# Kernel tuning notes

Measured on AMD Instinct MI355X. Metric: run time of the kernel, lower is better.

## Reference

```python
import jax, jax.numpy as jnp
import numpy as np

N = 262144  # num_channels (o*i)
K = 5       # kernel_size


def setup_inputs() -> dict:
    key = jax.random.key(0)
    k1, k2, k3 = jax.random.split(key, 3)
    return {
        "input_filter": jax.random.normal(k1, (N, K, K, K), dtype=jnp.float32),
        "theta_v": jax.random.normal(k2, (N, 3), dtype=jnp.float32),
        "theta": jax.random.normal(k3, (N,), dtype=jnp.float32),
    }


def _rodrigues(theta_v, theta):
    # F.normalize(theta_v, p=2) with eps=1e-12
    norm = jnp.linalg.norm(theta_v, axis=-1, keepdims=True)
    v = theta_v / jnp.maximum(norm, 1e-12)
    vx, vy, vz = v[:, 0], v[:, 1], v[:, 2]
    z = jnp.zeros_like(vx)
    # skew-symmetric cross-product matrix m, shape (n,3,3)
    m = jnp.stack([z, -vz, vy,
                   vz, z, -vx,
                   -vy, vx, z], axis=-1).reshape(-1, 3, 3)
    s = jnp.sin(theta)[:, None, None]
    c = (1.0 - jnp.cos(theta))[:, None, None]
    I3 = jnp.eye(3, dtype=theta_v.dtype)
    return I3 + s * m + c * jnp.einsum('nij,njk->nik', m, m)


def _base_grid(k):
    # matches _get_base_grids: coord along axis i -> channel 0, j -> 1, l -> 2
    c = jnp.linspace(-1.0, 1.0, k, dtype=jnp.float32)
    gi, gj, gl = jnp.meshgrid(c, c, c, indexing='ij')
    return jnp.stack([gi, gj, gl], axis=-1).reshape(k * k * k, 3)  # (k^3, 3)


def _grid_sample_3d_zeros(vol, grid):
    # vol: (n, D, H, W); grid: (n, P, 3) in [-1,1], channels (x->W, y->H, z->D)
    # trilinear, align_corners=True, padding_mode='zeros'
    n, D, H, W = vol.shape
    x = (grid[..., 0] + 1.0) * 0.5 * (W - 1)
    y = (grid[..., 1] + 1.0) * 0.5 * (H - 1)
    z = (grid[..., 2] + 1.0) * 0.5 * (D - 1)
    x0f, y0f, z0f = jnp.floor(x), jnp.floor(y), jnp.floor(z)
    wx, wy, wz = x - x0f, y - y0f, z - z0f
    x0, y0, z0 = x0f.astype(jnp.int32), y0f.astype(jnp.int32), z0f.astype(jnp.int32)
    bidx = jnp.arange(n)[:, None]
    out = jnp.zeros(grid.shape[:-1], dtype=vol.dtype)
    for dz in (0, 1):
        for dy in (0, 1):
            for dx in (0, 1):
                zi, yi, xi = z0 + dz, y0 + dy, x0 + dx
                w = ((wz if dz else 1.0 - wz) *
                     (wy if dy else 1.0 - wy) *
                     (wx if dx else 1.0 - wx))
                inb = ((zi >= 0) & (zi < D) & (yi >= 0) & (yi < H) &
                       (xi >= 0) & (xi < W))
                v = vol[bidx,
                        jnp.clip(zi, 0, D - 1),
                        jnp.clip(yi, 0, H - 1),
                        jnp.clip(xi, 0, W - 1)]
                out = out + w * jnp.where(inb, v, jnp.zeros_like(v))
    return out


def reference(input_filter, theta_v, theta):
    n = theta_v.shape[0]
    k = input_filter.shape[-1]
    vol = input_filter.reshape(n, k, k, k)
    R = _rodrigues(theta_v, theta)                    # (n,3,3)
    base = _base_grid(k)                              # (k^3,3)
    grids = jnp.einsum('pj,njk->npk', base, R)        # (n,k^3,3) = base @ R
    out = _grid_sample_3d_zeros(vol, grids)           # (n,k^3)
    return out.reshape(input_filter.shape)
```

## Files before the change

kernel.cpp:

```cpp
#include <hip/hip_runtime.h>
#include <math.h>

#define KP    125
#define VOL7P 344
#define WPB   4
#define NF    8

typedef _Float16 half_t;
typedef half_t h2 __attribute__((ext_vector_type(2)));
typedef __fp16 fp16x2 __attribute__((ext_vector_type(2)));

static __device__ __forceinline__ h2 h2fma(h2 a, h2 b, h2 c) {
    return __builtin_elementwise_fma(a, b, c);
}
static __device__ __forceinline__ h2 cvt_pk(float a, float b) {
    fp16x2 t = __builtin_amdgcn_cvt_pkrtz(a, b);
    return __builtin_bit_cast(h2, t);
}
static __device__ __forceinline__ float rdlane(float v, int k) {
    return __builtin_bit_cast(float,
        __builtin_amdgcn_readlane(__builtin_bit_cast(int, v), k));
}

__global__ __launch_bounds__(WPB * 64) void fastrot_kernel(
    const float* __restrict__ vol,
    const float* __restrict__ theta_v,
    const float* __restrict__ theta,
    float* __restrict__ out)
{
    __shared__ __align__(16) unsigned int pad[WPB][2][VOL7P];

    const int lane = threadIdx.x & 63;
    const int ws   = __builtin_amdgcn_readfirstlane(threadIdx.x >> 6);
    const long long base = ((long long)blockIdx.x * WPB + ws) * NF;

    uint4* f0 = (uint4*)(&pad[ws][0][0]);
    uint4* f1 = (uint4*)(&pad[ws][1][0]);
    const uint4 z4 = make_uint4(0u, 0u, 0u, 0u);
    f0[lane] = z4;
    f1[lane] = z4;
    if (lane < (VOL7P / 4 - 64)) { f0[lane + 64] = z4; f1[lane + 64] = z4; }

    float r00, r01, r02, r10, r11, r12, r20, r21, r22;
    {
        const long long m = base + (lane & (NF - 1));
        const float ax = theta_v[m * 3 + 0];
        const float ay = theta_v[m * 3 + 1];
        const float az = theta_v[m * 3 + 2];
        const float th = theta[m];
        const float d2  = ax * ax + ay * ay + az * az;
        const float inv = rsqrtf(fmaxf(d2, 1e-24f));
        const float vx = ax * inv, vy = ay * inv, vz = az * inv;
        float s, cth;
        __sincosf(th, &s, &cth);
        const float c = 1.0f - cth;
        r00 = 1.0f - c * (vy * vy + vz * vz);
        r01 = -s * vz + c * (vx * vy);
        r02 =  s * vy + c * (vx * vz);
        r10 =  s * vz + c * (vx * vy);
        r11 = 1.0f - c * (vx * vx + vz * vz);
        r12 = -s * vx + c * (vy * vz);
        r20 = -s * vy + c * (vx * vz);
        r21 =  s * vx + c * (vy * vz);
        r22 = 1.0f - c * (vx * vx + vy * vy);
    }

    const int p0 = lane;
    const int p1 = 124 - lane;
    const int i0 = (p0 * 41) >> 10;
    const int q0 = (p0 * 205) >> 10;
    const int j0 = q0 - i0 * 5;
    const int l0 = p0 - q0 * 5;
    const int i1 = 4 - i0, j1 = 4 - j0, l1 = 4 - l0;
    const int e0 = i0 * 49 + j0 * 7 + l0 + 57;
    const int e1 = i1 * 49 + j1 * 7 + l1 + 57;
    const float Bi0 = (float)(i0 - 2), Bj0 = (float)(j0 - 2), Bl0 = (float)(l0 - 2);

    float fv0[NF], fv1[NF], nx0[NF], nx1[NF];
#pragma unroll
    for (int k = 0; k < NF; ++k) {
        const float* vn = vol + (base + k) * KP;
        fv0[k] = vn[p0];
        fv1[k] = vn[p1];
        nx0[k] = (l0 < 4) ? vn[p0 + 1] : 0.0f;
        nx1[k] = (l1 < 4) ? vn[p1 + 1] : 0.0f;
    }

#pragma unroll
    for (int k = 0; k < NF; ++k) {
        unsigned int* buf = &pad[ws][k & 1][0];

        const float R00 = rdlane(r00, k), R01 = rdlane(r01, k), R02 = rdlane(r02, k);
        const float R10 = rdlane(r10, k), R11 = rdlane(r11, k), R12 = rdlane(r12, k);
        const float R20 = rdlane(r20, k), R21 = rdlane(r21, k), R22 = rdlane(r22, k);

        buf[e0] = __builtin_bit_cast(unsigned int, cvt_pk(fv0[k], nx0[k]));
        if (l0 == 0)
            buf[e0 - 1] = __builtin_bit_cast(unsigned int, cvt_pk(0.0f, fv0[k]));
        buf[e1] = __builtin_bit_cast(unsigned int, cvt_pk(fv1[k], nx1[k]));
        if (l1 == 0)
            buf[e1 - 1] = __builtin_bit_cast(unsigned int, cvt_pk(0.0f, fv1[k]));

        float* on = out + (base + k) * KP;

        const float xr = fmaf(Bi0, R00, fmaf(Bj0, R10, fmaf(Bl0, R20, 3.0f)));
        const float yr = fmaf(Bi0, R01, fmaf(Bj0, R11, fmaf(Bl0, R21, 3.0f)));
        const float zr = fmaf(Bi0, R02, fmaf(Bj0, R12, fmaf(Bl0, R22, 3.0f)));

        auto gather = [&](float xf, float yf, float zf) -> float {
            xf = fminf(fmaxf(xf, 0.0f), 5.99993896f);
            yf = fminf(fmaxf(yf, 0.0f), 5.99993896f);
            zf = fminf(fmaxf(zf, 0.0f), 5.99993896f);
            const int x0 = (int)xf, y0 = (int)yf, z0 = (int)zf;
            const float wx = __builtin_amdgcn_fractf(xf);
            const float wy = __builtin_amdgcn_fractf(yf);
            const float wz = __builtin_amdgcn_fractf(zf);
            const int ci = z0 * 49 + y0 * 7 + x0;

            const h2 A0 = __builtin_bit_cast(h2, buf[ci]);
            const h2 A1 = __builtin_bit_cast(h2, buf[ci + 49]);
            const h2 B0 = __builtin_bit_cast(h2, buf[ci + 7]);
            const h2 B1 = __builtin_bit_cast(h2, buf[ci + 56]);

            const h2 wzh = cvt_pk(wz, wz);
            const h2 wyh = cvt_pk(wy, wy);
            const h2 E = h2fma(wzh, A1 - A0, A0);
            const h2 F = h2fma(wzh, B1 - B0, B0);
            const h2 G = h2fma(wyh, F - E, E);
            const float g0 = (float)G.x;
            const float g1 = (float)G.y;
            return fmaf(wx, g1 - g0, g0);
        };

        on[p0] = gather(xr, yr, zr);
        on[p1] = gather(6.0f - xr, 6.0f - yr, 6.0f - zr);
    }
}

extern "C" void kernel_launch(void* const* d_in, const int* in_sizes, int n_in,
                              void* d_out, int out_size, void* d_ws, size_t ws_size,
                              hipStream_t stream) {
    const float* vol     = (const float*)d_in[0];
    const float* theta_v = (const float*)d_in[1];
    const float* theta   = (const float*)d_in[2];
    float* out           = (float*)d_out;

    const int N = in_sizes[2];

    fastrot_kernel<<<N / (WPB * NF), WPB * 64, 0, stream>>>(vol, theta_v, theta, out);
}
```

Before: 52.70 us.

## Pack 2x2 x-y neighbor quads into 64-bit LDS entries to halve gather loads

The LDS padded volume changes from a 7^3 grid of packed-half pairs to a 6^3 grid of uint2 entries, each holding the (x, x+1) pair for rows y and y+1. Each trilinear gather now does two 64-bit LDS reads instead of four 32-bit reads. In exchange, each channel needs four global loads per point instead of two, and the fill adds extra conditional boundary stores for the j==0 and l==0 faces. These changes raise the cost of staging data into LDS.

```diff
diff --git a/kernel.cpp b/kernel.cpp
--- a/kernel.cpp
+++ b/kernel.cpp
@@ -2,7 +2,7 @@
 #include <math.h>
 
 #define KP    125
-#define VOL7P 344
+#define NQE   252
 #define WPB   4
 #define NF    8
 
@@ -13,9 +13,16 @@
 static __device__ __forceinline__ h2 h2fma(h2 a, h2 b, h2 c) {
     return __builtin_elementwise_fma(a, b, c);
 }
+static __device__ __forceinline__ unsigned int cvt_pk_u(float a, float b) {
+    fp16x2 t = __builtin_amdgcn_cvt_pkrtz(a, b);
+    return __builtin_bit_cast(unsigned int, t);
+}
 static __device__ __forceinline__ h2 cvt_pk(float a, float b) {
     fp16x2 t = __builtin_amdgcn_cvt_pkrtz(a, b);
     return __builtin_bit_cast(h2, t);
+}
+static __device__ __forceinline__ h2 bch2(unsigned int u) {
+    return __builtin_bit_cast(h2, u);
 }
 static __device__ __forceinline__ float rdlane(float v, int k) {
     return __builtin_bit_cast(float,
@@ -28,18 +35,18 @@
     const float* __restrict__ theta,
     float* __restrict__ out)
 {
-    __shared__ __align__(16) unsigned int pad[WPB][2][VOL7P];
+    __shared__ __align__(16) uint2 pad[WPB][2][NQE];
 
     const int lane = threadIdx.x & 63;
     const int ws   = __builtin_amdgcn_readfirstlane(threadIdx.x >> 6);
     const long long base = ((long long)blockIdx.x * WPB + ws) * NF;
 
-    uint4* f0 = (uint4*)(&pad[ws][0][0]);
-    uint4* f1 = (uint4*)(&pad[ws][1][0]);
+    uint4* fp4 = (uint4*)(&pad[ws][0][0]);
     const uint4 z4 = make_uint4(0u, 0u, 0u, 0u);
-    f0[lane] = z4;
-    f1[lane] = z4;
-    if (lane < (VOL7P / 4 - 64)) { f0[lane + 64] = z4; f1[lane + 64] = z4; }
+    fp4[lane]       = z4;
+    fp4[lane + 64]  = z4;
+    fp4[lane + 128] = z4;
+    if (lane < 60) fp4[lane + 192] = z4;
 
     float r00, r01, r02, r10, r11, r12, r20, r21, r22;
     {
@@ -72,34 +79,59 @@
     const int j0 = q0 - i0 * 5;
     const int l0 = p0 - q0 * 5;
     const int i1 = 4 - i0, j1 = 4 - j0, l1 = 4 - l0;
-    const int e0 = i0 * 49 + j0 * 7 + l0 + 57;
-    const int e1 = i1 * 49 + j1 * 7 + l1 + 57;
     const float Bi0 = (float)(i0 - 2), Bj0 = (float)(j0 - 2), Bl0 = (float)(l0 - 2);
 
-    float fv0[NF], fv1[NF], nx0[NF], nx1[NF];
+    const int e0m = (i0 + 1) * 36 + (j0 + 1) * 6 + (l0 + 1);
+    const int e0x = (i0 + 1) * 36 + (j0 + 1) * 6;
+    const int e0y = (i0 + 1) * 36 + (l0 + 1);
+    const int e0c = (i0 + 1) * 36;
+    const int e1m = (i1 + 1) * 36 + (j1 + 1) * 6 + (l1 + 1);
+    const int e1x = (i1 + 1) * 36 + (j1 + 1) * 6;
+    const int e1y = (i1 + 1) * 36 + (l1 + 1);
+    const int e1c = (i1 + 1) * 36;
+
+    unsigned int s0x[NF], s0y[NF], s1x[NF], s1y[NF];
+    const int a1b = (p1 + 1 > 124) ? 124 : p1 + 1;
+    const int a1c = (p1 + 5 > 124) ? 124 : p1 + 5;
+    const int a1d = (p1 + 6 > 124) ? 124 : p1 + 6;
 #pragma unroll
     for (int k = 0; k < NF; ++k) {
         const float* vn = vol + (base + k) * KP;
-        fv0[k] = vn[p0];
-        fv1[k] = vn[p1];
-        nx0[k] = (l0 < 4) ? vn[p0 + 1] : 0.0f;
-        nx1[k] = (l1 < 4) ? vn[p1 + 1] : 0.0f;
+        float a = vn[p0];
+        float b = vn[p0 + 1];
+        float c = vn[p0 + 5];
+        float d = vn[p0 + 6];
+        if (l0 == 4) { b = 0.0f; d = 0.0f; }
+        if (j0 == 4) { c = 0.0f; d = 0.0f; }
+        s0x[k] = cvt_pk_u(a, b);
+        s0y[k] = cvt_pk_u(c, d);
+
+        float a1 = vn[p1];
+        float b1 = vn[a1b];
+        float c1 = vn[a1c];
+        float d1 = vn[a1d];
+        if (l1 == 4) { b1 = 0.0f; d1 = 0.0f; }
+        if (j1 == 4) { c1 = 0.0f; d1 = 0.0f; }
+        s1x[k] = cvt_pk_u(a1, b1);
+        s1y[k] = cvt_pk_u(c1, d1);
     }
 
 #pragma unroll
     for (int k = 0; k < NF; ++k) {
-        unsigned int* buf = &pad[ws][k & 1][0];
+        uint2* buf = &pad[ws][k & 1][0];
 
         const float R00 = rdlane(r00, k), R01 = rdlane(r01, k), R02 = rdlane(r02, k);
         const float R10 = rdlane(r10, k), R11 = rdlane(r11, k), R12 = rdlane(r12, k);
         const float R20 = rdlane(r20, k), R21 = rdlane(r21, k), R22 = rdlane(r22, k);
 
-        buf[e0] = __builtin_bit_cast(unsigned int, cvt_pk(fv0[k], nx0[k]));
-        if (l0 == 0)
-            buf[e0 - 1] = __builtin_bit_cast(unsigned int, cvt_pk(0.0f, fv0[k]));
-        buf[e1] = __builtin_bit_cast(unsigned int, cvt_pk(fv1[k], nx1[k]));
-        if (l1 == 0)
-            buf[e1 - 1] = __builtin_bit_cast(unsigned int, cvt_pk(0.0f, fv1[k]));
+        buf[e0m] = make_uint2(s0x[k], s0y[k]);
+        if (l0 == 0) buf[e0x] = make_uint2(s0x[k] << 16, s0y[k] << 16);
+        if (j0 == 0) buf[e0y] = make_uint2(0u, s0x[k]);
+        if (l0 == 0 && j0 == 0) buf[e0c] = make_uint2(0u, s0x[k] << 16);
+        buf[e1m] = make_uint2(s1x[k], s1y[k]);
+        if (l1 == 0) buf[e1x] = make_uint2(s1x[k] << 16, s1y[k] << 16);
+        if (j1 == 0) buf[e1y] = make_uint2(0u, s1x[k]);
+        if (l1 == 0 && j1 == 0) buf[e1c] = make_uint2(0u, s1x[k] << 16);
 
         float* on = out + (base + k) * KP;
 
@@ -115,18 +147,18 @@
             const float wx = __builtin_amdgcn_fractf(xf);
             const float wy = __builtin_amdgcn_fractf(yf);
             const float wz = __builtin_amdgcn_fractf(zf);
-            const int ci = z0 * 49 + y0 * 7 + x0;
+            const int ci8 = z0 * 36 + y0 * 6 + x0;
 
-            const h2 A0 = __builtin_bit_cast(h2, buf[ci]);
-            const h2 A1 = __builtin_bit_cast(h2, buf[ci + 49]);
-            const h2 B0 = __builtin_bit_cast(h2, buf[ci + 7]);
-            const h2 B1 = __builtin_bit_cast(h2, buf[ci + 56]);
+            const uint2 H0 = buf[ci8];
+            const uint2 H1 = buf[ci8 + 36];
+            const h2 lo0 = bch2(H0.x), hi0 = bch2(H0.y);
+            const h2 lo1 = bch2(H1.x), hi1 = bch2(H1.y);
 
             const h2 wzh = cvt_pk(wz, wz);
             const h2 wyh = cvt_pk(wy, wy);
-            const h2 E = h2fma(wzh, A1 - A0, A0);
-            const h2 F = h2fma(wzh, B1 - B0, B0);
-            const h2 G = h2fma(wyh, F - E, E);
+            const h2 E  = h2fma(wzh, lo1 - lo0, lo0);
+            const h2 Fh = h2fma(wzh, hi1 - hi0, hi0);
+            const h2 G  = h2fma(wyh, Fh - E, E);
             const float g0 = (float)G.x;
             const float g1 = (float)G.y;
             return fmaf(wx, g1 - g0, g0);
```

Measured after the change: 59.89 us. 1.14x slower.
